# Performance work log

Measured on AMD Instinct MI355X. Metric: run time of the kernel, lower is better.

## Reference

```python
import jax, jax.numpy as jnp
import numpy as np

BG_OPACITY = 1e10  # background_opacity
BG_COLOR = 0.0     # bg_color = (0.0,)


def setup_inputs() -> dict:
    key = jax.random.key(0)
    k1, k2, k3, k4 = jax.random.split(key, 4)
    B, R, N, C = 8, 16384, 128, 3
    rays_densities = jax.random.uniform(k1, (B, R, N, 1), dtype=jnp.float32) * 2.0
    rays_features = jax.random.uniform(k2, (B, R, N, C), dtype=jnp.float32)
    # monotonically increasing sample depths along the ray
    steps = jax.random.uniform(k3, (B, R, N), dtype=jnp.float32) * 0.05 + 0.01
    ray_lengths = jnp.cumsum(steps, axis=-1) + 2.0
    ray_directions = jax.random.normal(k4, (B, R, 3), dtype=jnp.float32)
    return {
        "rays_densities": rays_densities,
        "rays_features": rays_features,
        "ray_lengths": ray_lengths,
        "ray_directions": ray_directions,
    }


def reference(rays_densities, rays_features, ray_lengths, ray_directions):
    # deltas between consecutive samples; last delta is the background opacity
    deltas = jnp.concatenate(
        [ray_lengths[..., 1:] - ray_lengths[..., :-1],
         jnp.full_like(ray_lengths[..., :1], BG_OPACITY)], axis=-1)
    dir_norm = jnp.linalg.norm(ray_directions, axis=-1)  # (B, R)
    deltas = deltas * dir_norm[..., None]
    dens = jax.nn.relu(rays_densities[..., 0])  # density_relu=True, bias=0
    weighted = deltas * dens  # (B, R, N)
    capped = 1.0 - jnp.exp(-weighted)  # exponential capping
    rays_opacities = 1.0 - jnp.exp(-jnp.cumsum(weighted, axis=-1))
    opacities = rays_opacities[..., -1:]  # (B, R, 1)
    # roll absorption by surface_thickness=1 and set leading entry to 1
    absorption = 1.0 - rays_opacities
    absorption_shifted = jnp.roll(absorption, 1, axis=-1).at[..., :1].set(1.0)
    weights = capped * absorption_shifted  # product weight function
    depths = jnp.sum(weights * ray_lengths, axis=-1, keepdims=True)
    features = jnp.einsum('brn,brnc->brc', weights, rays_features)
    # blend_output=False -> alpha = 1; bg_color scalar 0.0 broadcast
    features = features + (1.0 - opacities) * BG_COLOR
    return features, depths, opacities, weights
```

## Files before the change

kernel.cpp:

```cpp
#include <hip/hip_runtime.h>


#define BG_OPACITY_F 1e10f

typedef float floatx4 __attribute__((ext_vector_type(4)));

__global__ __launch_bounds__(256) void ea_render_kernel(
    const float* __restrict__ dens,
    const float* __restrict__ feats,
    const float* __restrict__ lens,
    const float* __restrict__ dirs,
    float* __restrict__ out_feat,
    float* __restrict__ out_depth,
    float* __restrict__ out_opac,
    float* __restrict__ out_w,
    int n_rays)
{
    const int lane = threadIdx.x & 63;
    const int wave = threadIdx.x >> 6;
    const int g    = lane >> 4;
    const int t    = lane & 15;
    const long ray = (long)blockIdx.x * 16 + wave * 4 + g;
    if (ray >= n_rays) return;

    const long base = ray * 128;
    const int  n0   = t * 8;

    const float4 dA = *(const float4*)(dens + base + n0);
    const float4 dB = *(const float4*)(dens + base + n0 + 4);
    const float4 lA = *(const float4*)(lens + base + n0);
    const float4 lB = *(const float4*)(lens + base + n0 + 4);

    const float* fp = feats + base * 3 + (long)n0 * 3;
    const float4 f0 = *(const float4*)(fp +  0);
    const float4 f1 = *(const float4*)(fp +  4);
    const float4 f2 = *(const float4*)(fp +  8);
    const float4 f3 = *(const float4*)(fp + 12);
    const float4 f4 = *(const float4*)(fp + 16);
    const float4 f5 = *(const float4*)(fp + 20);

    const float* dp = dirs + ray * 3;
    const float dx = dp[0], dy = dp[1], dz = dp[2];
    const float dn = sqrtf(dx * dx + dy * dy + dz * dz);

    const float l[8]  = {lA.x, lA.y, lA.z, lA.w, lB.x, lB.y, lB.z, lB.w};
    const float dv[8] = {dA.x, dA.y, dA.z, dA.w, dB.x, dB.y, dB.z, dB.w};

    const float lnext = __shfl_down(lA.x, 1, 64);

    float w[8];
    #pragma unroll
    for (int i = 0; i < 7; ++i)
        w[i] = (l[i + 1] - l[i]) * dn * fmaxf(dv[i], 0.0f);
    const float delta7 = (t == 15) ? BG_OPACITY_F : (lnext - l[7]);
    w[7] = delta7 * dn * fmaxf(dv[7], 0.0f);
    const float w7s = (t == 15) ? 0.0f : w[7];

    const float s = w[0] + w[1] + w[2] + w[3] + w[4] + w[5] + w[6] + w7s;

    float inc = s;
    #pragma unroll
    for (int off = 1; off < 16; off <<= 1) {
        const float u = __shfl_up(inc, off, 64);
        if (t >= off) inc += u;
    }
    const float excl = inc - s;

    float a = __expf(-excl);
    float wgt[8];
    #pragma unroll
    for (int i = 0; i < 8; ++i) {
        const float ei = __expf(-w[i]);
        wgt[i] = (1.0f - ei) * a;
        a *= ei;
    }

    const float f[24] = {f0.x, f0.y, f0.z, f0.w, f1.x, f1.y, f1.z, f1.w,
                         f2.x, f2.y, f2.z, f2.w, f3.x, f3.y, f3.z, f3.w,
                         f4.x, f4.y, f4.z, f4.w, f5.x, f5.y, f5.z, f5.w};
    float pd = 0.0f, fr = 0.0f, fg = 0.0f, fb = 0.0f;
    #pragma unroll
    for (int i = 0; i < 8; ++i) {
        pd += wgt[i] * l[i];
        fr += wgt[i] * f[3 * i + 0];
        fg += wgt[i] * f[3 * i + 1];
        fb += wgt[i] * f[3 * i + 2];
    }

    #pragma unroll
    for (int off = 8; off; off >>= 1) {
        pd += __shfl_xor(pd, off, 64);
        fr += __shfl_xor(fr, off, 64);
        fg += __shfl_xor(fg, off, 64);
        fb += __shfl_xor(fb, off, 64);
    }

    const floatx4 wv0 = {wgt[0], wgt[1], wgt[2], wgt[3]};
    const floatx4 wv1 = {wgt[4], wgt[5], wgt[6], wgt[7]};
    __builtin_nontemporal_store(wv0, (floatx4*)(out_w + base + n0));
    __builtin_nontemporal_store(wv1, (floatx4*)(out_w + base + n0 + 4));

    if (t == 15) {
        out_opac[ray] = 1.0f - __expf(-(inc + w[7]));
    }
    if (t == 0) {
        out_feat[ray * 3 + 0] = fr;
        out_feat[ray * 3 + 1] = fg;
        out_feat[ray * 3 + 2] = fb;
        out_depth[ray] = pd;
    }
}

extern "C" void kernel_launch(void* const* d_in, const int* in_sizes, int n_in,
                              void* d_out, int out_size, void* d_ws, size_t ws_size,
                              hipStream_t stream) {
    const float* dens  = (const float*)d_in[0];
    const float* feats = (const float*)d_in[1];
    const float* lens  = (const float*)d_in[2];
    const float* dirs  = (const float*)d_in[3];

    const int n_rays = in_sizes[3] / 3;

    float* out = (float*)d_out;
    float* out_feat  = out;
    float* out_depth = out + (long)n_rays * 3;
    float* out_opac  = out + (long)n_rays * 4;
    float* out_w     = out + (long)n_rays * 5;

    const int blocks = (n_rays + 15) / 16;
    ea_render_kernel<<<blocks, 256, 0, stream>>>(
        dens, feats, lens, dirs, out_feat, out_depth, out_opac, out_w, n_rays);
}
```

Baseline: 380.8 us.

## Stage feature loads through LDS for fully coalesced global reads

Each block now loads its whole contiguous feature chunk with consecutive threads reading consecutive float4s, then transposes it through padded shared memory so each lane gets its 24 features. This replaces the per-lane strided 96-byte feature loads, which coalesce poorly. The weight and opacity stores move ahead of the barrier, and launch bounds request higher occupancy. The cost is extra LDS traffic, a block-wide barrier, and about 25 KB of shared memory per block, which may limit occupancy.

After: 381.1 us. About the same (+0.1%).

```diff
diff --git a/kernel.cpp b/kernel.cpp
--- a/kernel.cpp
+++ b/kernel.cpp
@@ -5,7 +5,9 @@
 
 typedef float floatx4 __attribute__((ext_vector_type(4)));
 
-__global__ __launch_bounds__(256) void ea_render_kernel(
+#define RSTRIDE 388
+
+__global__ __launch_bounds__(256, 4) void ea_render_kernel(
     const float* __restrict__ dens,
     const float* __restrict__ feats,
     const float* __restrict__ lens,
@@ -16,28 +18,32 @@
     float* __restrict__ out_w,
     int n_rays)
 {
-    const int lane = threadIdx.x & 63;
-    const int wave = threadIdx.x >> 6;
-    const int g    = lane >> 4;
+    __shared__ __align__(16) float sfeat[16 * RSTRIDE];
+
+    const int tid  = threadIdx.x;
+    const int lane = tid & 63;
     const int t    = lane & 15;
-    const long ray = (long)blockIdx.x * 16 + wave * 4 + g;
-    if (ray >= n_rays) return;
+    const int rb   = tid >> 4;
+    const long ray0 = (long)blockIdx.x * 16;
+    const long ray = (ray0 + rb < n_rays) ? (ray0 + rb) : (n_rays - 1);
 
     const long base = ray * 128;
     const int  n0   = t * 8;
+
+    const float* fblock = feats + ray0 * 384;
+    float4 fc[6];
+    #pragma unroll
+    for (int k = 0; k < 6; ++k) {
+        const int c = k * 256 + tid;
+        const bool ok = (ray0 + c / 96) < n_rays;
+        fc[k] = ok ? *(const float4*)(fblock + (long)c * 4)
+                   : make_float4(0.f, 0.f, 0.f, 0.f);
+    }
 
     const float4 dA = *(const float4*)(dens + base + n0);
     const float4 dB = *(const float4*)(dens + base + n0 + 4);
     const float4 lA = *(const float4*)(lens + base + n0);
     const float4 lB = *(const float4*)(lens + base + n0 + 4);
-
-    const float* fp = feats + base * 3 + (long)n0 * 3;
-    const float4 f0 = *(const float4*)(fp +  0);
-    const float4 f1 = *(const float4*)(fp +  4);
-    const float4 f2 = *(const float4*)(fp +  8);
-    const float4 f3 = *(const float4*)(fp + 12);
-    const float4 f4 = *(const float4*)(fp + 16);
-    const float4 f5 = *(const float4*)(fp + 20);
 
     const float* dp = dirs + ray * 3;
     const float dx = dp[0], dy = dp[1], dz = dp[2];
@@ -75,9 +81,37 @@
         a *= ei;
     }
 
-    const float f[24] = {f0.x, f0.y, f0.z, f0.w, f1.x, f1.y, f1.z, f1.w,
-                         f2.x, f2.y, f2.z, f2.w, f3.x, f3.y, f3.z, f3.w,
-                         f4.x, f4.y, f4.z, f4.w, f5.x, f5.y, f5.z, f5.w};
+    const floatx4 wv0 = {wgt[0], wgt[1], wgt[2], wgt[3]};
+    const floatx4 wv1 = {wgt[4], wgt[5], wgt[6], wgt[7]};
+    __builtin_nontemporal_store(wv0, (floatx4*)(out_w + base + n0));
+    __builtin_nontemporal_store(wv1, (floatx4*)(out_w + base + n0 + 4));
+
+    if (t == 15) {
+        out_opac[ray] = 1.0f - __expf(-(inc + w[7]));
+    }
+
+    #pragma unroll
+    for (int k = 0; k < 6; ++k) {
+        const int c   = k * 256 + tid;
+        const int r   = c / 96;
+        const int rem = c - r * 96;
+        const int tq  = rem / 6;
+        const int iq  = rem - tq * 6;
+        *(float4*)&sfeat[r * RSTRIDE + tq * 24 + iq * 4] = fc[k];
+    }
+    __syncthreads();
+
+    const float* myf = &sfeat[rb * RSTRIDE + t * 24];
+    const float4 q0 = *(const float4*)(myf +  0);
+    const float4 q1 = *(const float4*)(myf +  4);
+    const float4 q2 = *(const float4*)(myf +  8);
+    const float4 q3 = *(const float4*)(myf + 12);
+    const float4 q4 = *(const float4*)(myf + 16);
+    const float4 q5 = *(const float4*)(myf + 20);
+    const float f[24] = {q0.x, q0.y, q0.z, q0.w, q1.x, q1.y, q1.z, q1.w,
+                         q2.x, q2.y, q2.z, q2.w, q3.x, q3.y, q3.z, q3.w,
+                         q4.x, q4.y, q4.z, q4.w, q5.x, q5.y, q5.z, q5.w};
+
     float pd = 0.0f, fr = 0.0f, fg = 0.0f, fb = 0.0f;
     #pragma unroll
     for (int i = 0; i < 8; ++i) {
@@ -95,14 +129,6 @@
         fb += __shfl_xor(fb, off, 64);
     }
 
-    const floatx4 wv0 = {wgt[0], wgt[1], wgt[2], wgt[3]};
-    const floatx4 wv1 = {wgt[4], wgt[5], wgt[6], wgt[7]};
-    __builtin_nontemporal_store(wv0, (floatx4*)(out_w + base + n0));
-    __builtin_nontemporal_store(wv1, (floatx4*)(out_w + base + n0 + 4));
-
-    if (t == 15) {
-        out_opac[ray] = 1.0f - __expf(-(inc + w[7]));
-    }
     if (t == 0) {
         out_feat[ray * 3 + 0] = fr;
         out_feat[ray * 3 + 1] = fg;
```
